# Performance work log

Hardware: AMD Instinct MI355X
Metric: run time of the kernel (lower is better)

Reference implementation:

```python
import jax, jax.numpy as jnp
import numpy as np

B, T, D = 1, 2048, 3072
N, K, H = 16, 8, 256  # heads, kv heads, head dim
SOFT_CAP = 50.0
WINDOW = 1024
ROPE_BASE = 10000.0
ROPE_SCALE = 1.0
K_MASK = -2.3819763e+38
EPS = 1e-6


def rms_norm(x, scale=None):
    var = jnp.mean(jnp.square(x), axis=-1, keepdims=True)
    y = x * jax.lax.rsqrt(var + EPS)
    if scale is not None:
        y = y * (1.0 + scale)
    return y


def apply_rope(x, positions):
    # x: [B, T, n, H], positions: [B, T] int
    half = x.shape[-1] // 2
    fraction = 2.0 * jnp.arange(half, dtype=jnp.float32) / x.shape[-1]
    timescale = ROPE_BASE ** fraction  # [half]
    sinusoid = positions[..., None].astype(jnp.float32) / timescale  # [B,T,half]
    sinusoid = sinusoid[..., None, :] / ROPE_SCALE  # [B,T,1,half]
    sin, cos = jnp.sin(sinusoid), jnp.cos(sinusoid)
    first, second = jnp.split(x, 2, axis=-1)
    out = jnp.concatenate([first * cos - second * sin,
                           second * cos + first * sin], axis=-1)
    return out.astype(x.dtype)


def setup_inputs() -> dict:
    key = jax.random.key(0)
    ks = jax.random.split(key, 6)
    x = jax.random.normal(ks[0], (B, T, D), jnp.float32)
    segment_pos = jnp.broadcast_to(jnp.arange(T, dtype=jnp.int32), (B, T))
    attn_mask = jnp.broadcast_to(jnp.tril(jnp.ones((T, T), bool)), (B, T, T))
    w_q = jax.random.normal(ks[1], (N, D, H), jnp.float32) * 0.02
    w_kv = jax.random.normal(ks[2], (2, K, D, H), jnp.float32) * 0.02
    w_out = jax.random.normal(ks[3], (N, H, D), jnp.float32) * 0.02
    q_scale = jax.random.normal(ks[4], (H,), jnp.float32) * 0.1
    k_scale = jax.random.normal(ks[5], (H,), jnp.float32) * 0.1
    return {"x": x, "segment_pos": segment_pos, "attn_mask": attn_mask,
            "w_q": w_q, "w_kv": w_kv, "w_out": w_out,
            "q_scale": q_scale, "k_scale": k_scale}


def reference(x, segment_pos, attn_mask, w_q, w_kv, w_out, q_scale, k_scale):
    # Q projection + QK-RMSNorm + RoPE
    q = jnp.einsum('BTD,NDH->BTNH', x, w_q)
    q = rms_norm(q, q_scale)
    q = apply_rope(q, segment_pos)
    # fused KV projection
    kv = jnp.einsum('BSD,CKDH->CBSKH', x, w_kv)
    k_proj, v_proj = kv[0], kv[1]
    k_proj = rms_norm(k_proj, k_scale)
    v_proj = rms_norm(v_proj)  # value norm has no scale
    k_proj = apply_rope(k_proj, segment_pos)
    # GQA logits: q [B,T,K,G,H] x k [B,S,K,H]
    G = N // K
    qg = q.reshape(B, T, K, G, H)
    logits = jnp.einsum('BTKGH,BSKH->BTKGS', qg, k_proj).reshape(B, T, N, T)
    # logit soft-capping
    logits = jnp.tanh(logits / SOFT_CAP) * SOFT_CAP
    # sliding-window mask (cache_positions == segment_pos since cache is None)
    pos_q = segment_pos[:, :, None]
    pos_k = segment_pos[:, None, :]
    sliding = (pos_k > pos_q - WINDOW) & (pos_k < pos_q + WINDOW)  # [B,T,S]
    mask = attn_mask & sliding
    padded = jnp.where(mask[:, :, None, :], logits, K_MASK)
    probs = jax.nn.softmax(padded, axis=-1).astype(k_proj.dtype)
    enc = jnp.einsum('BTKGS,BSKH->BTKGH',
                     probs.reshape(B, T, K, G, T), v_proj).reshape(B, T, N, H)
    attn_output = jnp.einsum('BTNH,NHD->BTD', enc, w_out)
    return attn_output
```

## Files before the change

### kernel.cpp

```cpp
#include <hip/hip_runtime.h>
#include <math.h>

#define T_SEQ 2048
#define D_MODEL 3072
#define NQ 16
#define NKV 8
#define HD 256
#define NHEADS_TOT 32
#define QKV_COLS 8192
#define SOFT_CAP 50.0f
#define WINDOW 1024
#define K_MASK -2.3819763e38f

typedef __attribute__((ext_vector_type(8))) short bf16x8;
typedef __attribute__((ext_vector_type(4))) float f32x4;

__device__ __forceinline__ unsigned short f2bf(float f) {
    union { float f; unsigned u; } v; v.f = f;
    unsigned r = (v.u + 0x7fff + ((v.u >> 16) & 1)) >> 16;
    return (unsigned short)r;
}
__device__ __forceinline__ float bf2f(unsigned short u) {
    union { unsigned u; float f; } v; v.u = ((unsigned)u) << 16;
    return v.f;
}

__device__ __forceinline__ void gl_lds16(const unsigned short* g, unsigned short* l) {
    __builtin_amdgcn_global_load_lds(
        (const __attribute__((address_space(1))) void*)g,
        (__attribute__((address_space(3))) void*)l, 16, 0, 0);
}

__global__ __launch_bounds__(256) void k_convert(const float* __restrict__ src,
                                                 unsigned short* __restrict__ dst, int n4) {
    int i = blockIdx.x * 256 + threadIdx.x;
    if (i >= n4) return;
    float4 v = ((const float4*)src)[i];
    ushort4 o;
    o.x = f2bf(v.x); o.y = f2bf(v.y); o.z = f2bf(v.z); o.w = f2bf(v.w);
    ((ushort4*)dst)[i] = o;
}

__global__ __launch_bounds__(256) void k_transpose_bf16(const float* __restrict__ src,
                                                        unsigned short* __restrict__ dst,
                                                        int R, int C) {
    __shared__ float tile[32][33];
    int b = blockIdx.z;
    src += (size_t)b * R * C;
    dst += (size_t)b * R * C;
    int c0 = blockIdx.x * 32, r0 = blockIdx.y * 32;
    int tx = threadIdx.x, ty = threadIdx.y;
    #pragma unroll
    for (int i = ty; i < 32; i += 8)
        tile[i][tx] = src[(size_t)(r0 + i) * C + c0 + tx];
    __syncthreads();
    #pragma unroll
    for (int i = ty; i < 32; i += 8)
        dst[(size_t)(c0 + i) * R + r0 + tx] = f2bf(tile[tx][i]);
}

template <int OUT_BF16>
__global__ __launch_bounds__(256) void k_gemm_nt(const unsigned short* __restrict__ A,
                                                 const unsigned short* __restrict__ BT,
                                                 void* __restrict__ Cout,
                                                 int M, int N, int Kd) {
    __shared__ unsigned short As[128 * 64];
    __shared__ unsigned short Bs[128 * 64];
    const int tid = threadIdx.x;
    const int wave = tid >> 6, lane = tid & 63;
    const int col = lane & 15, quad = lane >> 4;
    const int wr = wave >> 1, wc = wave & 1;

    const int gx = M >> 7;
    int p = blockIdx.x;
    int xcd = p & 7, q = p >> 3;
    int i_t = q % gx, jj = q / gx;
    int j_t = jj * 8 + xcd;
    const int m0 = i_t * 128, n0 = j_t * 128;

    const int sub = wave & 1, isB = wave >> 1;
    const unsigned short* srcBase = isB ? (BT + (size_t)(n0 + sub * 64) * Kd)
                                        : (A + (size_t)(m0 + sub * 64) * Kd);
    unsigned short* ldsBase = (isB ? Bs : As) + sub * 64 * 64;
    const int lrow = lane >> 3, lchk = lane & 7;
    int soff[8];
    #pragma unroll
    for (int s = 0; s < 8; s++) {
        int r = s * 8 + lrow;
        soff[s] = r * Kd + ((lchk ^ (r & 7)) * 8);
    }

    f32x4 acc[4][4];
    #pragma unroll
    for (int i = 0; i < 4; i++)
        #pragma unroll
        for (int j = 0; j < 4; j++)
            acc[i][j] = (f32x4){0.f, 0.f, 0.f, 0.f};

    const int sw = col & 7;

    for (int k0 = 0; k0 < Kd; k0 += 64) {
        #pragma unroll
        for (int s = 0; s < 8; s++)
            gl_lds16(srcBase + soff[s] + k0, ldsBase + s * 512);
        __syncthreads();

        #pragma unroll
        for (int kk = 0; kk < 2; kk++) {
            bf16x8 af[4], bfr[4];
            const int chko = ((kk * 4 + quad) ^ sw) * 8;
            #pragma unroll
            for (int i = 0; i < 4; i++)
                af[i] = *(const bf16x8*)&As[(wr * 64 + i * 16 + col) * 64 + chko];
            #pragma unroll
            for (int j = 0; j < 4; j++)
                bfr[j] = *(const bf16x8*)&Bs[(wc * 64 + j * 16 + col) * 64 + chko];
            #pragma unroll
            for (int i = 0; i < 4; i++)
                #pragma unroll
                for (int j = 0; j < 4; j++)
                    acc[i][j] = __builtin_amdgcn_mfma_f32_16x16x32_bf16(af[i], bfr[j], acc[i][j], 0, 0, 0);
        }
        __syncthreads();
    }

    #pragma unroll
    for (int i = 0; i < 4; i++) {
        int row = m0 + wr * 64 + i * 16 + quad * 4;
        #pragma unroll
        for (int j = 0; j < 4; j++) {
            int c = n0 + wc * 64 + j * 16 + col;
            #pragma unroll
            for (int r = 0; r < 4; r++) {
                float v = acc[i][j][r];
                if (OUT_BF16)
                    ((unsigned short*)Cout)[(size_t)(row + r) * N + c] = f2bf(v);
                else
                    ((float*)Cout)[(size_t)(row + r) * N + c] = v;
            }
        }
    }
}

__global__ __launch_bounds__(256) void k_norm_rope(const unsigned short* __restrict__ qkv,
                                                   const int* __restrict__ spos,
                                                   const float* __restrict__ qscale,
                                                   const float* __restrict__ kscale,
                                                   unsigned short* __restrict__ qh,
                                                   unsigned short* __restrict__ kh,
                                                   unsigned short* __restrict__ vT) {
    const int t = blockIdx.x, slot = blockIdx.y, h = threadIdx.x;
    float val = bf2f(qkv[(size_t)t * QKV_COLS + slot * HD + h]);
    float ss = val * val;
    #pragma unroll
    for (int m = 1; m < 64; m <<= 1) ss += __shfl_xor(ss, m, 64);
    __shared__ float wsum[4];
    __shared__ float ybuf[256];
    if ((h & 63) == 0) wsum[h >> 6] = ss;
    __syncthreads();
    float tot = wsum[0] + wsum[1] + wsum[2] + wsum[3];
    float y = val * rsqrtf(tot * (1.0f / 256.0f) + 1e-6f);
    if (slot < 16) y *= (1.0f + qscale[h]);
    else if (slot < 24) y *= (1.0f + kscale[h]);

    if (slot < 24) {
        ybuf[h] = y;
        __syncthreads();
        int hh = h & 127;
        float fr = (float)hh * (1.0f / 128.0f);
        float ts = __expf(fr * 9.210340371976184f);
        float ang = (float)spos[t] / ts;
        float sn = __sinf(ang), cs = __cosf(ang);
        float other = ybuf[(h < 128) ? (h + 128) : (h - 128)];
        float outv = (h < 128) ? (y * cs - other * sn) : (y * cs + other * sn);
        if (slot < 16)
            qh[((size_t)slot * T_SEQ + t) * HD + h] = f2bf(outv);
        else
            kh[((size_t)(slot - 16) * T_SEQ + t) * HD + h] = f2bf(outv);
    } else {
        vT[((size_t)(slot - 24) * HD + h) * T_SEQ + t] = f2bf(y);
    }
}

__global__ __launch_bounds__(256) void k_attn(const unsigned short* __restrict__ qh,
                                              const unsigned short* __restrict__ kh,
                                              const unsigned short* __restrict__ vT,
                                              unsigned short* __restrict__ enc) {
    __shared__ unsigned short Ks[32 * 256];
    __shared__ unsigned short Vs[256 * 32];
    __shared__ unsigned short Pl[4][16 * 40];

    const int tid = threadIdx.x;
    const int wave = tid >> 6, lane = tid & 63;
    const int col = lane & 15, quad = lane >> 4;
    const int kk = blockIdx.x;
    const int t0b = blockIdx.y * 32;
    const int headSel = wave & 1, rowSel = wave >> 1;
    const int n = kk * 2 + headSel;
    const int tw = t0b + rowSel * 16;

    const unsigned short* qp = qh + ((size_t)n * T_SEQ + tw) * HD;
    const unsigned short* kp = kh + (size_t)kk * T_SEQ * HD;
    const unsigned short* vp = vT + (size_t)kk * HD * T_SEQ;

    bf16x8 qf[8];
    #pragma unroll
    for (int c = 0; c < 8; c++)
        qf[c] = *(const bf16x8*)(qp + (size_t)col * HD + c * 32 + quad * 8);

    int preK[4], preV[4], ldsKo[4], ldsVo[4];
    #pragma unroll
    for (int i = 0; i < 4; i++) {
        int krow = 2 * (wave * 4 + i) + (lane >> 5);
        int kpos = lane & 31;
        preK[i] = krow * HD + ((kpos ^ (krow & 7)) * 8);
        ldsKo[i] = (wave * 4 + i) * 512;
        int vh = (wave * 4 + i) * 16 + (lane >> 2);
        int vpp = lane & 3;
        preV[i] = vh * T_SEQ + ((vpp ^ (vh & 3)) * 8);
        ldsVo[i] = (wave * 4 + i) * 512;
    }

    f32x4 o[16];
    #pragma unroll
    for (int h = 0; h < 16; h++) o[h] = (f32x4){0.f, 0.f, 0.f, 0.f};
    float lsum[4] = {0.f, 0.f, 0.f, 0.f};

    int s_begin = t0b - (WINDOW - 1);
    if (s_begin < 0) s_begin = 0;
    s_begin &= ~31;
    const int s_end = t0b + 32;

    for (int s0 = s_begin; s0 < s_end; s0 += 32) {
        #pragma unroll
        for (int i = 0; i < 4; i++)
            gl_lds16(kp + (size_t)s0 * HD + preK[i], &Ks[ldsKo[i]]);
        #pragma unroll
        for (int i = 0; i < 4; i++)
            gl_lds16(vp + (size_t)s0 + preV[i], &Vs[ldsVo[i]]);
        __syncthreads();

        f32x4 S0 = (f32x4){0.f, 0.f, 0.f, 0.f};
        f32x4 S1 = (f32x4){0.f, 0.f, 0.f, 0.f};
        #pragma unroll
        for (int c = 0; c < 8; c++) {
            bf16x8 kf = *(const bf16x8*)&Ks[(size_t)col * HD + (((c * 4 + quad) ^ (col & 7)) * 8)];
            S0 = __builtin_amdgcn_mfma_f32_16x16x32_bf16(qf[c], kf, S0, 0, 0, 0);
        }
        #pragma unroll
        for (int c = 0; c < 8; c++) {
            bf16x8 kf = *(const bf16x8*)&Ks[(size_t)(16 + col) * HD + (((c * 4 + quad) ^ (col & 7)) * 8)];
            S1 = __builtin_amdgcn_mfma_f32_16x16x32_bf16(qf[c], kf, S1, 0, 0, 0);
        }

        #pragma unroll
        for (int r = 0; r < 4; r++) {
            int t = tw + quad * 4 + r;
            int sA = s0 + col, sB = sA + 16;
            bool vA = (sA <= t) && (sA >= t - (WINDOW - 1));
            bool vB = (sB <= t) && (sB >= t - (WINDOW - 1));
            float eA = __expf(S0[r] * (2.0f / SOFT_CAP));
            float eB = __expf(S1[r] * (2.0f / SOFT_CAP));
            float rA = __builtin_amdgcn_rcpf(eA + 1.0f);
            float rB = __builtin_amdgcn_rcpf(eB + 1.0f);
            float pA = __expf(SOFT_CAP - 2.0f * SOFT_CAP * rA);
            float pB = __expf(SOFT_CAP - 2.0f * SOFT_CAP * rB);
            pA = vA ? pA : 0.0f;
            pB = vB ? pB : 0.0f;
            lsum[r] += pA + pB;
            Pl[wave][(quad * 4 + r) * 40 + col] = f2bf(pA);
            Pl[wave][(quad * 4 + r) * 40 + 16 + col] = f2bf(pB);
        }

        bf16x8 pf = *(const bf16x8*)&Pl[wave][col * 40 + quad * 8];

        #pragma unroll
        for (int ht = 0; ht < 16; ht++) {
            int h = ht * 16 + col;
            bf16x8 vf = *(const bf16x8*)&Vs[(size_t)h * 32 + ((quad ^ (h & 3)) * 8)];
            o[ht] = __builtin_amdgcn_mfma_f32_16x16x32_bf16(pf, vf, o[ht], 0, 0, 0);
        }
        __syncthreads();
    }

    #pragma unroll
    for (int r = 0; r < 4; r++) {
        #pragma unroll
        for (int m = 1; m < 16; m <<= 1)
            lsum[r] += __shfl_xor(lsum[r], m, 16);
        lsum[r] = 1.0f / lsum[r];
    }
    #pragma unroll
    for (int ht = 0; ht < 16; ht++) {
        #pragma unroll
        for (int r = 0; r < 4; r++) {
            int t = tw + quad * 4 + r;
            enc[(size_t)t * (NQ * HD) + n * HD + ht * 16 + col] = f2bf(o[ht][r] * lsum[r]);
        }
    }
}

extern "C" void kernel_launch(void* const* d_in, const int* in_sizes, int n_in,
                              void* d_out, int out_size, void* d_ws, size_t ws_size,
                              hipStream_t stream) {
    const float* x       = (const float*)d_in[0];
    const int*   spos    = (const int*)d_in[1];
    const float* w_q     = (const float*)d_in[3];
    const float* w_kv    = (const float*)d_in[4];
    const float* w_out   = (const float*)d_in[5];
    const float* q_scale = (const float*)d_in[6];
    const float* k_scale = (const float*)d_in[7];
    float* out = (float*)d_out;

    char* ws = (char*)d_ws;
    unsigned short* xb     = (unsigned short*)(ws + 0);
    unsigned short* wT     = (unsigned short*)(ws + 12582912);
    unsigned short* wToutb = (unsigned short*)(ws + 12582912);
    unsigned short* encb   = (unsigned short*)(ws + 37748736);
    unsigned short* qkv    = (unsigned short*)(ws + 62914560);
    unsigned short* qh     = (unsigned short*)(ws + 96468992);
    unsigned short* kh     = (unsigned short*)(ws + 113246208);
    unsigned short* vT     = (unsigned short*)(ws + 121634816);

    k_convert<<<dim3((T_SEQ * D_MODEL / 4 + 255) / 256), dim3(256), 0, stream>>>(
        x, xb, T_SEQ * D_MODEL / 4);
    k_transpose_bf16<<<dim3(HD / 32, D_MODEL / 32, NQ), dim3(32, 8), 0, stream>>>(
        w_q, wT, D_MODEL, HD);
    k_transpose_bf16<<<dim3(HD / 32, D_MODEL / 32, 16), dim3(32, 8), 0, stream>>>(
        w_kv, wT + (size_t)4096 * D_MODEL, D_MODEL, HD);
    k_gemm_nt<1><<<dim3((T_SEQ / 128) * (QKV_COLS / 128)), dim3(256), 0, stream>>>(
        xb, wT, qkv, T_SEQ, QKV_COLS, D_MODEL);
    k_transpose_bf16<<<dim3(D_MODEL / 32, 4096 / 32, 1), dim3(32, 8), 0, stream>>>(
        w_out, wToutb, 4096, D_MODEL);
    k_norm_rope<<<dim3(T_SEQ, NHEADS_TOT), dim3(256), 0, stream>>>(
        qkv, spos, q_scale, k_scale, qh, kh, vT);
    k_attn<<<dim3(NKV, T_SEQ / 32), dim3(256), 0, stream>>>(qh, kh, vT, encb);
    k_gemm_nt<0><<<dim3((T_SEQ / 128) * (D_MODEL / 128)), dim3(256), 0, stream>>>(
        encb, wToutb, out, T_SEQ, D_MODEL, NQ * HD);
}
```

Baseline: 558.9 us.

## Widen attention key tile to 64 and transpose V in a separate kernel

The attention loop now processes 64 keys per iteration instead of 32. Each iteration issues twice the K/V loads and runs four score MFMA groups plus two PV MFMAs per head tile, which halves the number of barrier syncs per block. The norm/rope kernel now writes V row-major with coalesced stores, and a new shared-memory transpose kernel produces the V-transposed layout, replacing the strided scattered stores. The cost is doubled LDS use (about 73KB), which may lower occupancy, plus one extra launch and an extra pass over V. Aligning the start to 64 also adds some wasted masked work at the window edge.

After: 550.1 us. No clear change (-1.6%).

```diff
diff --git a/kernel.cpp b/kernel.cpp
--- a/kernel.cpp
+++ b/kernel.cpp
@@ -57,6 +57,23 @@
     #pragma unroll
     for (int i = ty; i < 32; i += 8)
         dst[(size_t)(c0 + i) * R + r0 + tx] = f2bf(tile[tx][i]);
+}
+
+__global__ __launch_bounds__(256) void k_transpose_v(const unsigned short* __restrict__ src,
+                                                     unsigned short* __restrict__ dst) {
+    __shared__ unsigned short tile[32][34];
+    int kk = blockIdx.z;
+    src += (size_t)kk * T_SEQ * HD;
+    dst += (size_t)kk * HD * T_SEQ;
+    int h0 = blockIdx.x * 32, t0 = blockIdx.y * 32;
+    int tx = threadIdx.x, ty = threadIdx.y;
+    #pragma unroll
+    for (int i = ty; i < 32; i += 8)
+        tile[i][tx] = src[(size_t)(t0 + i) * HD + h0 + tx];
+    __syncthreads();
+    #pragma unroll
+    for (int i = ty; i < 32; i += 8)
+        dst[(size_t)(h0 + i) * T_SEQ + t0 + tx] = tile[tx][i];
 }
 
 template <int OUT_BF16>
@@ -148,7 +165,7 @@
                                                    const float* __restrict__ kscale,
                                                    unsigned short* __restrict__ qh,
                                                    unsigned short* __restrict__ kh,
-                                                   unsigned short* __restrict__ vT) {
+                                                   unsigned short* __restrict__ vh) {
     const int t = blockIdx.x, slot = blockIdx.y, h = threadIdx.x;
     float val = bf2f(qkv[(size_t)t * QKV_COLS + slot * HD + h]);
     float ss = val * val;
@@ -178,7 +195,7 @@
         else
             kh[((size_t)(slot - 16) * T_SEQ + t) * HD + h] = f2bf(outv);
     } else {
-        vT[((size_t)(slot - 24) * HD + h) * T_SEQ + t] = f2bf(y);
+        vh[((size_t)(slot - 24) * T_SEQ + t) * HD + h] = f2bf(y);
     }
 }
 
@@ -186,9 +203,9 @@
                                               const unsigned short* __restrict__ kh,
                                               const unsigned short* __restrict__ vT,
                                               unsigned short* __restrict__ enc) {
-    __shared__ unsigned short Ks[32 * 256];
-    __shared__ unsigned short Vs[256 * 32];
-    __shared__ unsigned short Pl[4][16 * 40];
+    __shared__ unsigned short Ks[64 * 256];
+    __shared__ unsigned short Vs[256 * 64];
+    __shared__ unsigned short Pl[4][16 * 72];
 
     const int tid = threadIdx.x;
     const int wave = tid >> 6, lane = tid & 63;
@@ -208,17 +225,16 @@
     for (int c = 0; c < 8; c++)
         qf[c] = *(const bf16x8*)(qp + (size_t)col * HD + c * 32 + quad * 8);
 
-    int preK[4], preV[4], ldsKo[4], ldsVo[4];
-    #pragma unroll
-    for (int i = 0; i < 4; i++) {
-        int krow = 2 * (wave * 4 + i) + (lane >> 5);
-        int kpos = lane & 31;
-        preK[i] = krow * HD + ((kpos ^ (krow & 7)) * 8);
-        ldsKo[i] = (wave * 4 + i) * 512;
-        int vh = (wave * 4 + i) * 16 + (lane >> 2);
-        int vpp = lane & 3;
-        preV[i] = vh * T_SEQ + ((vpp ^ (vh & 3)) * 8);
-        ldsVo[i] = (wave * 4 + i) * 512;
+    int preK[8], preV[8];
+    #pragma unroll
+    for (int i = 0; i < 8; i++) {
+        int j = wave * 8 + i;
+        int krow = 2 * j + (lane >> 5);
+        int kg = lane & 31;
+        preK[i] = krow * HD + ((kg ^ (krow & 7)) * 8);
+        int vrow = 8 * j + (lane >> 3);
+        int vg = lane & 7;
+        preV[i] = vrow * T_SEQ + ((vg ^ (vrow & 7)) * 8);
     }
 
     f32x4 o[16];
@@ -228,57 +244,58 @@
 
     int s_begin = t0b - (WINDOW - 1);
     if (s_begin < 0) s_begin = 0;
-    s_begin &= ~31;
+    s_begin &= ~63;
     const int s_end = t0b + 32;
 
-    for (int s0 = s_begin; s0 < s_end; s0 += 32) {
-        #pragma unroll
-        for (int i = 0; i < 4; i++)
-            gl_lds16(kp + (size_t)s0 * HD + preK[i], &Ks[ldsKo[i]]);
-        #pragma unroll
-        for (int i = 0; i < 4; i++)
-            gl_lds16(vp + (size_t)s0 + preV[i], &Vs[ldsVo[i]]);
-        __syncthreads();
-
-        f32x4 S0 = (f32x4){0.f, 0.f, 0.f, 0.f};
-        f32x4 S1 = (f32x4){0.f, 0.f, 0.f, 0.f};
-        #pragma unroll
-        for (int c = 0; c < 8; c++) {
-            bf16x8 kf = *(const bf16x8*)&Ks[(size_t)col * HD + (((c * 4 + quad) ^ (col & 7)) * 8)];
-            S0 = __builtin_amdgcn_mfma_f32_16x16x32_bf16(qf[c], kf, S0, 0, 0, 0);
-        }
-        #pragma unroll
-        for (int c = 0; c < 8; c++) {
-            bf16x8 kf = *(const bf16x8*)&Ks[(size_t)(16 + col) * HD + (((c * 4 + quad) ^ (col & 7)) * 8)];
-            S1 = __builtin_amdgcn_mfma_f32_16x16x32_bf16(qf[c], kf, S1, 0, 0, 0);
-        }
+    for (int s0 = s_begin; s0 < s_end; s0 += 64) {
+        #pragma unroll
+        for (int i = 0; i < 8; i++)
+            gl_lds16(kp + (size_t)s0 * HD + preK[i], &Ks[(wave * 8 + i) * 512]);
+        #pragma unroll
+        for (int i = 0; i < 8; i++)
+            gl_lds16(vp + (size_t)s0 + preV[i], &Vs[(wave * 8 + i) * 512]);
+        __syncthreads();
+
+        f32x4 S[4];
+        #pragma unroll
+        for (int g = 0; g < 4; g++) S[g] = (f32x4){0.f, 0.f, 0.f, 0.f};
+        #pragma unroll
+        for (int g = 0; g < 4; g++)
+            #pragma unroll
+            for (int c = 0; c < 8; c++) {
+                bf16x8 kf = *(const bf16x8*)&Ks[(size_t)(g * 16 + col) * 256 +
+                                                (((c * 4 + quad) ^ (col & 7)) * 8)];
+                S[g] = __builtin_amdgcn_mfma_f32_16x16x32_bf16(qf[c], kf, S[g], 0, 0, 0);
+            }
 
         #pragma unroll
         for (int r = 0; r < 4; r++) {
             int t = tw + quad * 4 + r;
-            int sA = s0 + col, sB = sA + 16;
-            bool vA = (sA <= t) && (sA >= t - (WINDOW - 1));
-            bool vB = (sB <= t) && (sB >= t - (WINDOW - 1));
-            float eA = __expf(S0[r] * (2.0f / SOFT_CAP));
-            float eB = __expf(S1[r] * (2.0f / SOFT_CAP));
-            float rA = __builtin_amdgcn_rcpf(eA + 1.0f);
-            float rB = __builtin_amdgcn_rcpf(eB + 1.0f);
-            float pA = __expf(SOFT_CAP - 2.0f * SOFT_CAP * rA);
-            float pB = __expf(SOFT_CAP - 2.0f * SOFT_CAP * rB);
-            pA = vA ? pA : 0.0f;
-            pB = vB ? pB : 0.0f;
-            lsum[r] += pA + pB;
-            Pl[wave][(quad * 4 + r) * 40 + col] = f2bf(pA);
-            Pl[wave][(quad * 4 + r) * 40 + 16 + col] = f2bf(pB);
-        }
-
-        bf16x8 pf = *(const bf16x8*)&Pl[wave][col * 40 + quad * 8];
+            float p[4];
+            #pragma unroll
+            for (int g = 0; g < 4; g++) {
+                int s = s0 + g * 16 + col;
+                bool vld = (s <= t) && (s >= t - (WINDOW - 1));
+                float e = __expf(S[g][r] * (2.0f / SOFT_CAP));
+                float rc = __builtin_amdgcn_rcpf(e + 1.0f);
+                float pv = __expf(SOFT_CAP - 2.0f * SOFT_CAP * rc);
+                p[g] = vld ? pv : 0.0f;
+                Pl[wave][(quad * 4 + r) * 72 + g * 16 + col] = f2bf(p[g]);
+            }
+            lsum[r] += p[0] + p[1];
+            lsum[r] += p[2] + p[3];
+        }
+
+        bf16x8 pf0 = *(const bf16x8*)&Pl[wave][col * 72 + quad * 8];
+        bf16x8 pf1 = *(const bf16x8*)&Pl[wave][col * 72 + 32 + quad * 8];
 
         #pragma unroll
         for (int ht = 0; ht < 16; ht++) {
             int h = ht * 16 + col;
-            bf16x8 vf = *(const bf16x8*)&Vs[(size_t)h * 32 + ((quad ^ (h & 3)) * 8)];
-            o[ht] = __builtin_amdgcn_mfma_f32_16x16x32_bf16(pf, vf, o[ht], 0, 0, 0);
+            bf16x8 vf0 = *(const bf16x8*)&Vs[(size_t)h * 64 + ((quad ^ (h & 7)) * 8)];
+            bf16x8 vf1 = *(const bf16x8*)&Vs[(size_t)h * 64 + (((quad + 4) ^ (h & 7)) * 8)];
+            o[ht] = __builtin_amdgcn_mfma_f32_16x16x32_bf16(pf0, vf0, o[ht], 0, 0, 0);
+            o[ht] = __builtin_amdgcn_mfma_f32_16x16x32_bf16(pf1, vf1, o[ht], 0, 0, 0);
         }
         __syncthreads();
     }
@@ -314,6 +331,7 @@
 
     char* ws = (char*)d_ws;
     unsigned short* xb     = (unsigned short*)(ws + 0);
+    unsigned short* vh     = (unsigned short*)(ws + 0);
     unsigned short* wT     = (unsigned short*)(ws + 12582912);
     unsigned short* wToutb = (unsigned short*)(ws + 12582912);
     unsigned short* encb   = (unsigned short*)(ws + 37748736);
@@ -333,7 +351,8 @@
     k_transpose_bf16<<<dim3(D_MODEL / 32, 4096 / 32, 1), dim3(32, 8), 0, stream>>>(
         w_out, wToutb, 4096, D_MODEL);
     k_norm_rope<<<dim3(T_SEQ, NHEADS_TOT), dim3(256), 0, stream>>>(
-        qkv, spos, q_scale, k_scale, qh, kh, vT);
+        qkv, spos, q_scale, k_scale, qh, kh, vh);
+    k_transpose_v<<<dim3(HD / 32, T_SEQ / 32, NKV), dim3(32, 8), 0, stream>>>(vh, vT);
     k_attn<<<dim3(NKV, T_SEQ / 32), dim3(256), 0, stream>>>(qh, kh, vT, encb);
     k_gemm_nt<0><<<dim3((T_SEQ / 128) * (D_MODEL / 128)), dim3(256), 0, stream>>>(
         encb, wToutb, out, T_SEQ, D_MODEL, NQ * HD);
```
